# Optimization experiments

Hardware: AMD Instinct MI355X
Metric: run time of the kernel (lower is better)

## Reference

```python
import jax, jax.numpy as jnp
from jax import lax
import numpy as np

K_SIZE = 3  # deformable kernel size
PAD = 1
STRIDE = 1


def _conv3x3(x, w, b):
    # plain 3x3 conv, pad 1, stride 1, NCHW/OIHW
    y = lax.conv_general_dilated(x, w, window_strides=(1, 1),
                                 padding=[(1, 1), (1, 1)],
                                 dimension_numbers=('NCHW', 'OIHW', 'NCHW'))
    return y + b[None, :, None, None]


def _deform_sample(x, py, px):
    """Bilinear sample x [B,C,H,W] at float coords py,px [B,K,Ho,Wo].
    Out-of-bounds samples contribute zero (matches torchvision deform_conv2d).
    Returns [B,C,K,Ho,Wo]."""
    B, C, H, W = x.shape
    y0 = jnp.floor(py)
    x0 = jnp.floor(px)
    gat = jax.vmap(lambda img, iy, ix: img[:, iy, ix])  # per-batch gather -> [C,K,Ho,Wo]
    out = jnp.zeros((B, C) + py.shape[1:], dtype=x.dtype)
    for yc, xc in ((y0, x0), (y0, x0 + 1), (y0 + 1, x0), (y0 + 1, x0 + 1)):
        wgt = (1.0 - jnp.abs(py - yc)) * (1.0 - jnp.abs(px - xc))
        valid = (yc >= 0) & (yc <= H - 1) & (xc >= 0) & (xc <= W - 1)
        wgt = jnp.where(valid, wgt, 0.0)
        iy = jnp.clip(yc, 0, H - 1).astype(jnp.int32)
        ix = jnp.clip(xc, 0, W - 1).astype(jnp.int32)
        out = out + wgt[:, None] * gat(x, iy, ix)
    return out


def reference(x, w_off, b_off, w_mask, b_mask, w_dcn, b_dcn):
    k = K_SIZE
    K = k * k
    B, C, H, W = x.shape
    # offset conv (2*K channels: (dy, dx) pairs per kernel position, row-major)
    offset = _conv3x3(x, w_off, b_off)            # [B, 2K, H, W]
    mask = jax.nn.sigmoid(_conv3x3(x, w_mask, b_mask))  # [B, K, H, W]
    off = offset.reshape(B, K, 2, H, W)
    dy, dx = off[:, :, 0], off[:, :, 1]
    ki = (jnp.arange(K) // k).astype(x.dtype)  # kernel row index
    kj = (jnp.arange(K) % k).astype(x.dtype)   # kernel col index
    # sampling coordinates: out position * stride - pad + kernel pos + learned offset
    py = (jnp.arange(H, dtype=x.dtype)[None, None, :, None] * STRIDE - PAD
          + ki[None, :, None, None] + dy)
    px = (jnp.arange(W, dtype=x.dtype)[None, None, None, :] * STRIDE - PAD
          + kj[None, :, None, None] + dx)
    val = _deform_sample(x, py, px) * mask[:, None]   # [B,C,K,H,W]
    Cout = w_dcn.shape[0]
    out = jnp.einsum('ock,bckhw->bohw', w_dcn.reshape(Cout, C, K), val)
    return out + b_dcn[None, :, None, None]


def setup_inputs() -> dict:
    key = jax.random.key(0)
    ks = jax.random.split(key, 6)
    B, C, Cout, H, W, k = 4, 256, 256, 64, 64, 3
    K = k * k
    x = jax.random.normal(ks[0], (B, C, H, W), dtype=jnp.float32)
    # NOTE: original inits offset/mask conv to zeros (degenerate -> plain conv).
    # Use small random weights so offsets/masks are nontrivial but local.
    w_off = jax.random.normal(ks[1], (2 * K, C, 3, 3), dtype=jnp.float32) * 0.01
    b_off = jnp.zeros((2 * K,), dtype=jnp.float32)
    w_mask = jax.random.normal(ks[2], (K, C, 3, 3), dtype=jnp.float32) * 0.01
    b_mask = jnp.zeros((K,), dtype=jnp.float32)
    fan_in = C * K
    w_dcn = jax.random.normal(ks[3], (Cout, C, 3, 3), dtype=jnp.float32) / np.sqrt(fan_in)
    b_dcn = jnp.zeros((Cout,), dtype=jnp.float32)
    return {"x": x, "w_off": w_off, "b_off": b_off, "w_mask": w_mask,
            "b_mask": b_mask, "w_dcn": w_dcn, "b_dcn": b_dcn}
```

## Files before the change

kernel.cpp:

```cpp
#include <hip/hip_runtime.h>
#include <math.h>

#define B_ 4
#define C_ 256
#define CO_ 256
#define H_ 64
#define W_ 64
#define HW_ 4096
#define KK_ 9
#define NCH_ 27

typedef __attribute__((ext_vector_type(8))) short bf16x8;
typedef __attribute__((ext_vector_type(4))) float f32x4;

__device__ inline unsigned short f32_to_bf16(float f) {
    unsigned int u = __float_as_uint(f);
    unsigned int r = (u + 0x7FFFu + ((u >> 16) & 1u)) >> 16;
    return (unsigned short)r;
}

__global__ void prep_all(const float* __restrict__ x, unsigned short* __restrict__ xTh,
                         const float* __restrict__ w_dcn, const float* __restrict__ w_off,
                         const float* __restrict__ w_mask,
                         unsigned short* __restrict__ wTs, unsigned short* __restrict__ wCs) {
    __shared__ float tile[32][33];
    __shared__ float lw[2304];
    const int t = threadIdx.x;
    const int bid = blockIdx.x;
    if (bid < 4096) {
        const int tx = t & 31, ty = t >> 5;
        const int b = bid >> 10;
        const int rem = bid & 1023;
        const int c0 = (rem >> 7) << 5;
        const int hw0 = (rem & 127) << 5;
        const float* xb = x + ((size_t)b << 20);
        unsigned short* xTb = xTh + ((size_t)b << 20);
#pragma unroll
        for (int r = 0; r < 4; ++r) {
            int row = ty + (r << 3);
            tile[row][tx] = xb[((size_t)(c0 + row) << 12) + hw0 + tx];
        }
        __syncthreads();
#pragma unroll
        for (int r = 0; r < 4; ++r) {
            int row = ty + (r << 3);
            xTb[((size_t)(hw0 + row) << 8) + c0 + tx] = f32_to_bf16(tile[tx][row]);
        }
    } else if (bid < 4352) {
        const int o = bid - 4096;
        for (int e = t; e < 2304; e += 256) lw[e] = w_dcn[(size_t)o * 2304 + e];
        __syncthreads();
        for (int e = t; e < 2304; e += 256) {
            int k = e >> 8, c = e & 255;
            int chunk = (k << 2) + (c >> 6), ck = c & 63;
            int pos = (o << 6) + (((ck >> 3) ^ (o & 7)) << 3) + (ck & 7);
            wTs[(size_t)chunk * 16384 + pos] = f32_to_bf16(lw[c * 9 + k]);
        }
    } else {
        const int ch = bid - 4352;
        const float* src = (ch < 18) ? w_off + (size_t)ch * 2304
                         : (ch < NCH_) ? w_mask + (size_t)(ch - 18) * 2304
                         : nullptr;
        for (int e = t; e < 2304; e += 256) lw[e] = src ? src[e] : 0.f;
        __syncthreads();
        for (int e = t; e < 2304; e += 256) {
            int k = e >> 8, c = e & 255;
            int chunk = (k << 2) + (c >> 6), ck = c & 63;
            int pos = (ch << 6) + (((ck >> 3) ^ (ch & 7)) << 3) + (ck & 7);
            wCs[(size_t)chunk * 2048 + pos] = f32_to_bf16(lw[c * 9 + k]);
        }
    }
}

__global__ __launch_bounds__(256, 2) void conv_mfma(
    const unsigned short* __restrict__ xTh, const unsigned short* __restrict__ wCs,
    const float* __restrict__ b_off, const float* __restrict__ b_mask,
    float* __restrict__ offmask) {
    __shared__ alignas(16) unsigned short wlds[2][2048];
    __shared__ alignas(16) unsigned short xlds[2][2048];
    const int t = threadIdx.x;
    const int bid = blockIdx.x;
    const int b = (bid & 7) >> 1;
    const int ph = bid & 1;
    const int hh = bid >> 3;
    const unsigned short* xb = xTh + ((size_t)b << 20);

    auto stage_w = [&](int chunk, int buf) {
        const unsigned short* g = wCs + ((size_t)chunk << 11) + (t << 3);
        __builtin_amdgcn_global_load_lds(
            (const __attribute__((address_space(1))) unsigned int*)g,
            (__attribute__((address_space(3))) unsigned int*)&wlds[buf][t << 3], 16, 0, 0);
    };

    auto stage_x = [&](int chunk, int buf) {
        int k = chunk >> 2, cc = chunk & 3;
        int ki = k / 3, kj = k % 3;
        int py = hh + ki - 1;
        int p = t >> 3, cs = t & 7;
        int px = (ph << 5) + p + kj - 1;
        uint4 u = make_uint4(0u, 0u, 0u, 0u);
        if (py >= 0 && py < H_ && px >= 0 && px < W_)
            u = *(const uint4*)(xb + (((size_t)((py << 6) + px)) << 8) + (cc << 6) + (cs << 3));
        *(uint4*)&xlds[buf][(p << 6) + ((cs ^ (p & 7)) << 3)] = u;
    };

    const int wid = t >> 6, lane = t & 63;
    const int wc = wid >> 1, wp = wid & 1;
    const int m16 = lane & 15, kg = lane >> 4;
    f32x4 acc = {};

    stage_w(0, 0);
    stage_x(0, 0);
    __syncthreads();

    for (int chunk = 0; chunk < 36; ++chunk) {
        int cur = chunk & 1, nxt = cur ^ 1;
        if (chunk < 35) { stage_w(chunk + 1, nxt); stage_x(chunk + 1, nxt); }
#pragma unroll
        for (int ks = 0; ks < 2; ++ks) {
            int s = (ks << 2) + kg;
            int o = (wc << 4) + m16;
            bf16x8 a = *(const bf16x8*)&wlds[cur][(o << 6) + ((s ^ (o & 7)) << 3)];
            int p = (wp << 4) + m16;
            bf16x8 bf = *(const bf16x8*)&xlds[cur][(p << 6) + ((s ^ (p & 7)) << 3)];
            acc = __builtin_amdgcn_mfma_f32_16x16x32_bf16(a, bf, acc, 0, 0, 0);
        }
        __syncthreads();
    }

    const int pix = (hh << 6) + (ph << 5) + (wp << 4) + m16;
#pragma unroll
    for (int r = 0; r < 4; ++r) {
        int ch = (wc << 4) + (kg << 2) + r;
        if (ch < NCH_) {
            float bias = (ch < 18) ? b_off[ch] : b_mask[ch - 18];
            offmask[(((size_t)b * NCH_ + ch) << 12) + pix] = acc[r] + bias;
        }
    }
}

__global__ __launch_bounds__(512, 4) void dcn_fused(
    const unsigned short* __restrict__ xTh, const float* __restrict__ offmask,
    const unsigned short* __restrict__ wTs, float* __restrict__ part) {
    __shared__ ushort4 cwh[576];
    __shared__ uchar4 coffb[576];
    __shared__ alignas(16) unsigned short wbuf[2][16384];
    __shared__ alignas(16) unsigned short vbuf[4096];

    const int t = threadIdx.x;
    const int bid = blockIdx.x;
    const int b = (bid & 7) >> 1;
    const int half = bid & 1;
    const int tile64 = bid >> 3;
    const int pix0 = tile64 << 6;
    const unsigned short* xb = xTh + ((size_t)b << 20);
    const float* omb = offmask + (((size_t)b * NCH_) << 12);

    for (int e = t; e < 576; e += 512) {
        int k = e >> 6, p = e & 63;
        int pix = pix0 + p;
        int hh = pix >> 6, ww = pix & 63;
        float dy = omb[((size_t)(2 * k) << 12) + pix];
        float dx = omb[((size_t)(2 * k + 1) << 12) + pix];
        float ml = omb[((size_t)(18 + k) << 12) + pix];
        float m = 1.f / (1.f + __expf(-ml));
        float py = (float)(hh - 1 + (k / 3)) + dy;
        float px = (float)(ww - 1 + (k % 3)) + dx;
        float fy0 = floorf(py), fx0 = floorf(px);
        float ay = py - fy0, ax = px - fx0;
        bool y0v = (fy0 >= 0.f) && (fy0 <= 63.f);
        bool y1v = (fy0 >= -1.f) && (fy0 <= 62.f);
        bool x0v = (fx0 >= 0.f) && (fx0 <= 63.f);
        bool x1v = (fx0 >= -1.f) && (fx0 <= 62.f);
        int y0 = (int)fy0, x0 = (int)fx0;
        int iy0 = min(max(y0, 0), 63), iy1 = min(max(y0 + 1, 0), 63);
        int ix0 = min(max(x0, 0), 63), ix1 = min(max(x0 + 1, 0), 63);
        float w00 = (y0v && x0v) ? m * (1.f - ay) * (1.f - ax) : 0.f;
        float w01 = (y0v && x1v) ? m * (1.f - ay) * ax : 0.f;
        float w10 = (y1v && x0v) ? m * ay * (1.f - ax) : 0.f;
        float w11 = (y1v && x1v) ? m * ay * ax : 0.f;
        cwh[e] = make_ushort4(f32_to_bf16(w00), f32_to_bf16(w01),
                              f32_to_bf16(w10), f32_to_bf16(w11));
        coffb[e] = make_uchar4((unsigned char)iy0, (unsigned char)ix0,
                               (unsigned char)iy1, (unsigned char)ix1);
    }

    const int oct = t & 7, pq = t >> 3;
    const int wid = t >> 6, lane = t & 63;
    const int wo = wid >> 1, wp = wid & 1;
    const int m16 = lane & 15, kg = lane >> 4;
    const int vslot = (pq << 6) + ((oct ^ (pq & 7)) << 3);

    auto stage_w = [&](int c, int slot) {
        int gc = ((c >> 1) << 2) + (half << 1) + (c & 1);
#pragma unroll
        for (int r = 0; r < 4; ++r) {
            int off16 = (r << 9) + t;
            const unsigned short* g = wTs + ((size_t)gc << 14) + (off16 << 3);
            __builtin_amdgcn_global_load_lds(
                (const __attribute__((address_space(1))) unsigned int*)g,
                (__attribute__((address_space(3))) unsigned int*)&wbuf[slot][off16 << 3], 16, 0, 0);
        }
    };

    auto gather = [&](int c, uint4* g) {
        int k = c >> 1, cc = (half << 1) + (c & 1);
        uchar4 q = coffb[(k << 6) + pq];
        const unsigned short* cb = xb + (cc << 6) + (oct << 3);
        g[0] = *(const uint4*)(cb + ((((int)q.x << 6) + q.y) << 8));
        g[1] = *(const uint4*)(cb + ((((int)q.x << 6) + q.w) << 8));
        g[2] = *(const uint4*)(cb + ((((int)q.z << 6) + q.y) << 8));
        g[3] = *(const uint4*)(cb + ((((int)q.z << 6) + q.w) << 8));
    };

    auto finish = [&](int c, const uint4* g) {
        int k = c >> 1;
        ushort4 wv = cwh[(k << 6) + pq];
        float w0 = __uint_as_float((unsigned int)wv.x << 16);
        float w1 = __uint_as_float((unsigned int)wv.y << 16);
        float w2 = __uint_as_float((unsigned int)wv.z << 16);
        float w3 = __uint_as_float((unsigned int)wv.w << 16);
        union { uint4 v; unsigned int u[4]; } A, B2, C2, D2;
        A.v = g[0]; B2.v = g[1]; C2.v = g[2]; D2.v = g[3];
        unsigned int o4[4];
#pragma unroll
        for (int j = 0; j < 4; ++j) {
            float al = __uint_as_float(A.u[j] << 16);
            float ah = __uint_as_float(A.u[j] & 0xffff0000u);
            float bl = __uint_as_float(B2.u[j] << 16);
            float bh = __uint_as_float(B2.u[j] & 0xffff0000u);
            float cl = __uint_as_float(C2.u[j] << 16);
            float ch = __uint_as_float(C2.u[j] & 0xffff0000u);
            float dl = __uint_as_float(D2.u[j] << 16);
            float dh = __uint_as_float(D2.u[j] & 0xffff0000u);
            float vl = w0 * al + w1 * bl + w2 * cl + w3 * dl;
            float vh = w0 * ah + w1 * bh + w2 * ch + w3 * dh;
            unsigned int pk;
            asm("v_cvt_pk_bf16_f32 %0, %1, %2" : "=v"(pk) : "v"(vl), "v"(vh));
            o4[j] = pk;
        }
        *(uint4*)&vbuf[vslot] = make_uint4(o4[0], o4[1], o4[2], o4[3]);
    };

    f32x4 acc[4][2] = {};

    auto compute = [&](int slot) {
#pragma unroll
        for (int ks = 0; ks < 2; ++ks) {
            int s = (ks << 2) + kg;
            bf16x8 aF[4], bF[2];
#pragma unroll
            for (int i = 0; i < 4; ++i) {
                int o = (wo << 6) + (i << 4) + m16;
                aF[i] = *(const bf16x8*)&wbuf[slot][(o << 6) + ((s ^ (o & 7)) << 3)];
            }
#pragma unroll
            for (int j = 0; j < 2; ++j) {
                int p = (wp << 5) + (j << 4) + m16;
                bF[j] = *(const bf16x8*)&vbuf[(p << 6) + ((s ^ (p & 7)) << 3)];
            }
#pragma unroll
            for (int i = 0; i < 4; ++i)
#pragma unroll
                for (int j = 0; j < 2; ++j)
                    acc[i][j] = __builtin_amdgcn_mfma_f32_16x16x32_bf16(
                        aF[i], bF[j], acc[i][j], 0, 0, 0);
        }
    };

    uint4 gA[4], gB[4];

    __syncthreads();
    gather(0, gA);
    stage_w(0, 0);

#define HALFSTEP(CUR, GCUR, GNXT, NW1, NW2)                              \
    __builtin_amdgcn_s_barrier();                                        \
    asm volatile("" ::: "memory");                                       \
    if ((CUR) + 1 < 18) { gather((CUR) + 1, GNXT); stage_w((CUR) + 1, ((CUR) + 1) & 1); } \
    asm volatile("s_waitcnt vmcnt(" #NW1 ")" ::: "memory");              \
    finish((CUR), GCUR);                                                 \
    asm volatile("s_waitcnt vmcnt(" #NW2 ") lgkmcnt(0)" ::: "memory");   \
    __builtin_amdgcn_s_barrier();                                        \
    asm volatile("" ::: "memory");                                       \
    __builtin_amdgcn_s_setprio(1);                                       \
    compute((CUR) & 1);                                                  \
    __builtin_amdgcn_s_setprio(0);

    for (int c = 0; c < 16; c += 2) {
        HALFSTEP(c, gA, gB, 12, 8)
        HALFSTEP(c + 1, gB, gA, 12, 8)
    }
    HALFSTEP(16, gA, gB, 12, 8)
    HALFSTEP(17, gB, gA, 4, 0)
#undef HALFSTEP

    float* pd = part + (((size_t)((half << 2) + b)) << 20);
#pragma unroll
    for (int i = 0; i < 4; ++i) {
        int ob = (wo << 6) + (i << 4) + (kg << 2);
#pragma unroll
        for (int j = 0; j < 2; ++j) {
            int p = pix0 + (wp << 5) + (j << 4) + m16;
#pragma unroll
            for (int r = 0; r < 4; ++r) {
                int oo = ob + r;
                pd[(((size_t)oo) << 12) + p] = acc[i][j][r];
            }
        }
    }
}

__global__ __launch_bounds__(256) void combine_out(
    const float* __restrict__ part, const float* __restrict__ b_dcn,
    float* __restrict__ out) {
    int i = (blockIdx.x * 256 + threadIdx.x) << 3;
    float bias = b_dcn[(i >> 12) & 255];
    const float* p1 = part + ((size_t)4 << 20);
    float4 a0 = *(const float4*)(part + i);
    float4 a1 = *(const float4*)(part + i + 4);
    float4 c0 = *(const float4*)(p1 + i);
    float4 c1 = *(const float4*)(p1 + i + 4);
    float4 r0 = make_float4(a0.x + c0.x + bias, a0.y + c0.y + bias,
                            a0.z + c0.z + bias, a0.w + c0.w + bias);
    float4 r1 = make_float4(a1.x + c1.x + bias, a1.y + c1.y + bias,
                            a1.z + c1.z + bias, a1.w + c1.w + bias);
    *(float4*)(out + i) = r0;
    *(float4*)(out + i + 4) = r1;
}

extern "C" void kernel_launch(void* const* d_in, const int* in_sizes, int n_in,
                              void* d_out, int out_size, void* d_ws, size_t ws_size,
                              hipStream_t stream) {
    const float* x      = (const float*)d_in[0];
    const float* w_off  = (const float*)d_in[1];
    const float* b_off  = (const float*)d_in[2];
    const float* w_mask = (const float*)d_in[3];
    const float* b_mask = (const float*)d_in[4];
    const float* w_dcn  = (const float*)d_in[5];
    const float* b_dcn  = (const float*)d_in[6];
    float* out = (float*)d_out;

    float* ws = (float*)d_ws;
    float* offmask = ws;
    unsigned short* xTh = (unsigned short*)(offmask + (size_t)B_ * NCH_ * HW_);
    unsigned short* wTs = xTh + ((size_t)B_ * HW_ * C_);
    unsigned short* wCs = wTs + (size_t)36 * 16384;
    float* part = (float*)(wCs + (size_t)36 * 2048);

    prep_all<<<dim3(4384), dim3(256), 0, stream>>>(x, xTh, w_dcn, w_off, w_mask, wTs, wCs);
    conv_mfma<<<dim3(512), dim3(256), 0, stream>>>(xTh, wCs, b_off, b_mask, offmask);
    dcn_fused<<<dim3(512), dim3(512), 0, stream>>>(xTh, offmask, wTs, part);
    combine_out<<<dim3(2048), dim3(256), 0, stream>>>(part, b_dcn, out);
}
```

Before: 73.84 us.

## Triple-buffer offset conv, pack bilinear math, store partials as bf16

The offset/mask conv kernel moves to a three-slot LDS ring. Global x loads go into registers with clamped addresses, and one barrier per chunk replaces the previous double barrier scheme, so loads overlap MFMA. The bilinear interpolation in dcn_fused uses float2 vector math so the compiler can emit packed FMA. The split-K partial outputs are written as bf16 instead of fp32, halving partial-buffer traffic, at the cost of extra rounding error in the final output.

```diff
diff --git a/kernel.cpp b/kernel.cpp
--- a/kernel.cpp
+++ b/kernel.cpp
@@ -12,6 +12,7 @@
 
 typedef __attribute__((ext_vector_type(8))) short bf16x8;
 typedef __attribute__((ext_vector_type(4))) float f32x4;
+typedef __attribute__((ext_vector_type(2))) float f32x2;
 
 __device__ inline unsigned short f32_to_bf16(float f) {
     unsigned int u = __float_as_uint(f);
@@ -76,8 +77,8 @@
     const unsigned short* __restrict__ xTh, const unsigned short* __restrict__ wCs,
     const float* __restrict__ b_off, const float* __restrict__ b_mask,
     float* __restrict__ offmask) {
-    __shared__ alignas(16) unsigned short wlds[2][2048];
-    __shared__ alignas(16) unsigned short xlds[2][2048];
+    __shared__ alignas(16) unsigned short wlds[3][2048];
+    __shared__ alignas(16) unsigned short xlds[3][2048];
     const int t = threadIdx.x;
     const int bid = blockIdx.x;
     const int b = (bid & 7) >> 1;
@@ -85,23 +86,28 @@
     const int hh = bid >> 3;
     const unsigned short* xb = xTh + ((size_t)b << 20);
 
-    auto stage_w = [&](int chunk, int buf) {
+    auto stage_w = [&](int chunk, int slot) {
         const unsigned short* g = wCs + ((size_t)chunk << 11) + (t << 3);
         __builtin_amdgcn_global_load_lds(
             (const __attribute__((address_space(1))) unsigned int*)g,
-            (__attribute__((address_space(3))) unsigned int*)&wlds[buf][t << 3], 16, 0, 0);
-    };
-
-    auto stage_x = [&](int chunk, int buf) {
+            (__attribute__((address_space(3))) unsigned int*)&wlds[slot][t << 3], 16, 0, 0);
+    };
+
+    const int xp = t >> 3, xcs = t & 7;
+    uint4 xr;
+    bool xvalid;
+    auto xload = [&](int chunk) {
         int k = chunk >> 2, cc = chunk & 3;
         int ki = k / 3, kj = k % 3;
         int py = hh + ki - 1;
-        int p = t >> 3, cs = t & 7;
-        int px = (ph << 5) + p + kj - 1;
-        uint4 u = make_uint4(0u, 0u, 0u, 0u);
-        if (py >= 0 && py < H_ && px >= 0 && px < W_)
-            u = *(const uint4*)(xb + (((size_t)((py << 6) + px)) << 8) + (cc << 6) + (cs << 3));
-        *(uint4*)&xlds[buf][(p << 6) + ((cs ^ (p & 7)) << 3)] = u;
+        int px = (ph << 5) + xp + kj - 1;
+        xvalid = (py >= 0) & (py < H_) & (px >= 0) & (px < W_);
+        int pyc = min(max(py, 0), 63), pxc = min(max(px, 0), 63);
+        xr = *(const uint4*)(xb + (((size_t)((pyc << 6) + pxc)) << 8) + (cc << 6) + (xcs << 3));
+    };
+    auto xwrite = [&](int slot) {
+        uint4 u = xvalid ? xr : make_uint4(0u, 0u, 0u, 0u);
+        *(uint4*)&xlds[slot][(xp << 6) + ((xcs ^ (xp & 7)) << 3)] = u;
     };
 
     const int wid = t >> 6, lane = t & 63;
@@ -109,24 +115,38 @@
     const int m16 = lane & 15, kg = lane >> 4;
     f32x4 acc = {};
 
-    stage_w(0, 0);
-    stage_x(0, 0);
-    __syncthreads();
-
-    for (int chunk = 0; chunk < 36; ++chunk) {
-        int cur = chunk & 1, nxt = cur ^ 1;
-        if (chunk < 35) { stage_w(chunk + 1, nxt); stage_x(chunk + 1, nxt); }
+    auto compute = [&](int slot) {
 #pragma unroll
         for (int ks = 0; ks < 2; ++ks) {
             int s = (ks << 2) + kg;
             int o = (wc << 4) + m16;
-            bf16x8 a = *(const bf16x8*)&wlds[cur][(o << 6) + ((s ^ (o & 7)) << 3)];
+            bf16x8 a = *(const bf16x8*)&wlds[slot][(o << 6) + ((s ^ (o & 7)) << 3)];
             int p = (wp << 4) + m16;
-            bf16x8 bf = *(const bf16x8*)&xlds[cur][(p << 6) + ((s ^ (p & 7)) << 3)];
+            bf16x8 bf = *(const bf16x8*)&xlds[slot][(p << 6) + ((s ^ (p & 7)) << 3)];
             acc = __builtin_amdgcn_mfma_f32_16x16x32_bf16(a, bf, acc, 0, 0, 0);
         }
-        __syncthreads();
-    }
+    };
+
+    xload(0);
+    stage_w(0, 0);
+    asm volatile("s_waitcnt vmcnt(1)" ::: "memory");
+    xwrite(0);
+
+    for (int c = 0; c < 35; ++c) {
+        xload(c + 1);
+        stage_w(c + 1, (c + 1) % 3);
+        asm volatile("s_waitcnt vmcnt(1)" ::: "memory");
+        xwrite((c + 1) % 3);
+        asm volatile("s_waitcnt lgkmcnt(0)" ::: "memory");
+        __builtin_amdgcn_s_barrier();
+        asm volatile("" ::: "memory");
+        compute(c % 3);
+    }
+    asm volatile("s_waitcnt vmcnt(0)" ::: "memory");
+    asm volatile("s_waitcnt lgkmcnt(0)" ::: "memory");
+    __builtin_amdgcn_s_barrier();
+    asm volatile("" ::: "memory");
+    compute(35 % 3);
 
     const int pix = (hh << 6) + (ph << 5) + (wp << 4) + m16;
 #pragma unroll
@@ -141,7 +161,7 @@
 
 __global__ __launch_bounds__(512, 4) void dcn_fused(
     const unsigned short* __restrict__ xTh, const float* __restrict__ offmask,
-    const unsigned short* __restrict__ wTs, float* __restrict__ part) {
+    const unsigned short* __restrict__ wTs, unsigned short* __restrict__ part) {
     __shared__ ushort4 cwh[576];
     __shared__ uchar4 coffb[576];
     __shared__ alignas(16) unsigned short wbuf[2][16384];
@@ -225,18 +245,13 @@
         unsigned int o4[4];
 #pragma unroll
         for (int j = 0; j < 4; ++j) {
-            float al = __uint_as_float(A.u[j] << 16);
-            float ah = __uint_as_float(A.u[j] & 0xffff0000u);
-            float bl = __uint_as_float(B2.u[j] << 16);
-            float bh = __uint_as_float(B2.u[j] & 0xffff0000u);
-            float cl = __uint_as_float(C2.u[j] << 16);
-            float ch = __uint_as_float(C2.u[j] & 0xffff0000u);
-            float dl = __uint_as_float(D2.u[j] << 16);
-            float dh = __uint_as_float(D2.u[j] & 0xffff0000u);
-            float vl = w0 * al + w1 * bl + w2 * cl + w3 * dl;
-            float vh = w0 * ah + w1 * bh + w2 * ch + w3 * dh;
+            f32x2 a2 = {__uint_as_float(A.u[j] << 16),  __uint_as_float(A.u[j] & 0xffff0000u)};
+            f32x2 b2 = {__uint_as_float(B2.u[j] << 16), __uint_as_float(B2.u[j] & 0xffff0000u)};
+            f32x2 c2 = {__uint_as_float(C2.u[j] << 16), __uint_as_float(C2.u[j] & 0xffff0000u)};
+            f32x2 d2 = {__uint_as_float(D2.u[j] << 16), __uint_as_float(D2.u[j] & 0xffff0000u)};
+            f32x2 v2 = a2 * w0 + b2 * w1 + c2 * w2 + d2 * w3;
             unsigned int pk;
-            asm("v_cvt_pk_bf16_f32 %0, %1, %2" : "=v"(pk) : "v"(vl), "v"(vh));
+            asm("v_cvt_pk_bf16_f32 %0, %1, %2" : "=v"(pk) : "v"(v2.x), "v"(v2.y));
             o4[j] = pk;
         }
         *(uint4*)&vbuf[vslot] = make_uint4(o4[0], o4[1], o4[2], o4[3]);
@@ -295,7 +310,7 @@
     HALFSTEP(17, gB, gA, 4, 0)
 #undef HALFSTEP
 
-    float* pd = part + (((size_t)((half << 2) + b)) << 20);
+    unsigned short* pd = part + (((size_t)((half << 2) + b)) << 20);
 #pragma unroll
     for (int i = 0; i < 4; ++i) {
         int ob = (wo << 6) + (i << 4) + (kg << 2);
@@ -305,28 +320,32 @@
 #pragma unroll
             for (int r = 0; r < 4; ++r) {
                 int oo = ob + r;
-                pd[(((size_t)oo) << 12) + p] = acc[i][j][r];
+                pd[(((size_t)oo) << 12) + p] = f32_to_bf16(acc[i][j][r]);
             }
         }
     }
 }
 
 __global__ __launch_bounds__(256) void combine_out(
-    const float* __restrict__ part, const float* __restrict__ b_dcn,
+    const unsigned short* __restrict__ part, const float* __restrict__ b_dcn,
     float* __restrict__ out) {
     int i = (blockIdx.x * 256 + threadIdx.x) << 3;
     float bias = b_dcn[(i >> 12) & 255];
-    const float* p1 = part + ((size_t)4 << 20);
-    float4 a0 = *(const float4*)(part + i);
-    float4 a1 = *(const float4*)(part + i + 4);
-    float4 c0 = *(const float4*)(p1 + i);
-    float4 c1 = *(const float4*)(p1 + i + 4);
-    float4 r0 = make_float4(a0.x + c0.x + bias, a0.y + c0.y + bias,
-                            a0.z + c0.z + bias, a0.w + c0.w + bias);
-    float4 r1 = make_float4(a1.x + c1.x + bias, a1.y + c1.y + bias,
-                            a1.z + c1.z + bias, a1.w + c1.w + bias);
-    *(float4*)(out + i) = r0;
-    *(float4*)(out + i + 4) = r1;
+    union { uint4 v; unsigned int u[4]; } A, B2;
+    A.v  = *(const uint4*)(part + i);
+    B2.v = *(const uint4*)(part + ((size_t)4 << 20) + i);
+    float r[8];
+#pragma unroll
+    for (int j = 0; j < 4; ++j) {
+        float a_lo = __uint_as_float(A.u[j] << 16);
+        float a_hi = __uint_as_float(A.u[j] & 0xffff0000u);
+        float b_lo = __uint_as_float(B2.u[j] << 16);
+        float b_hi = __uint_as_float(B2.u[j] & 0xffff0000u);
+        r[2 * j]     = a_lo + b_lo + bias;
+        r[2 * j + 1] = a_hi + b_hi + bias;
+    }
+    *(float4*)(out + i)     = make_float4(r[0], r[1], r[2], r[3]);
+    *(float4*)(out + i + 4) = make_float4(r[4], r[5], r[6], r[7]);
 }
 
 extern "C" void kernel_launch(void* const* d_in, const int* in_sizes, int n_in,
@@ -346,7 +365,7 @@
     unsigned short* xTh = (unsigned short*)(offmask + (size_t)B_ * NCH_ * HW_);
     unsigned short* wTs = xTh + ((size_t)B_ * HW_ * C_);
     unsigned short* wCs = wTs + (size_t)36 * 16384;
-    float* part = (float*)(wCs + (size_t)36 * 2048);
+    unsigned short* part = wCs + (size_t)36 * 2048;
 
     prep_all<<<dim3(4384), dim3(256), 0, stream>>>(x, xTh, w_dcn, w_off, w_mask, wTs, wCs);
     conv_mfma<<<dim3(512), dim3(256), 0, stream>>>(xTh, wCs, b_off, b_mask, offmask);
```

Result: no change. 72.87 us, median of 2 (-1.3%).
